# Optimization experiments

Hardware: AMD Instinct MI355X
Metric: run time of the kernel (lower is better)

Reference implementation:

```python
import jax, jax.numpy as jnp
import numpy as np

NUM_CLASSES = 100000
FEAT_DIM = 512
BATCH = 32768
ALPHA1 = 1.0
ALPHA2 = 50.0  # alpha * 50
A_CONST = 0.2
WARMUP = 15
EPS = 1e-12  # torch F.normalize eps


def setup_inputs() -> dict:
    key = jax.random.key(0)
    k1, k2, k3, k4 = jax.random.split(key, 4)
    x = jax.random.normal(k1, (BATCH, FEAT_DIM), dtype=jnp.float32)
    labels = jax.random.randint(k2, (BATCH,), 0, NUM_CLASSES, dtype=jnp.int64)
    ori_labels = jax.random.randint(k3, (BATCH,), 0, NUM_CLASSES, dtype=jnp.int64)
    centers = jax.random.normal(k4, (NUM_CLASSES, FEAT_DIM), dtype=jnp.float32)
    return {"x": x, "labels": labels, "ori_labels": ori_labels, "epoch": 5, "centers": centers}


def _l2norm(v, axis):
    # matches torch F.normalize(p=2): divide by max(||v||, eps)
    n = jnp.sqrt(jnp.sum(v * v, axis=axis, keepdims=True))
    return v / jnp.maximum(n, EPS)


def reference(x, labels, ori_labels, epoch, centers):
    C = centers.shape[0]
    xn = _l2norm(x, axis=1)                      # [B, D]
    cn = _l2norm(centers, axis=1)                # [C, D]

    all_centers_mean = jnp.sum(cn, axis=0) / C   # [D]
    s_all = xn @ all_centers_mean                # [B]  dot(x, mean of all centers)

    # one-hot multiply-and-sum == direct gather of the label's center
    c_lab = cn[labels]                           # [B, D]
    s_lab = jnp.sum(c_lab * xn, axis=1)          # [B]

    e_all = jnp.exp(s_all)
    # first branch scales the gathered center by (C+1)/C before the dot
    loss_1 = jnp.mean((e_all - jnp.exp(s_lab * ((C + 1.0) / C))) / ALPHA1)
    loss_2 = jnp.mean(-jnp.abs((e_all - jnp.exp(s_lab) + A_CONST) / ALPHA2))

    v = min(epoch / (WARMUP - 1), 1)             # epoch is a Python int
    loss = (1.0 - v) * loss_1 + v * loss_2
    return (loss, centers)
```

## Files before the change

### kernel.cpp

```cpp
#include <hip/hip_runtime.h>
#include <math.h>

#define C_CLASSES 100000
#define FEAT      512
#define BATCH_N   32768
#define EPS_N     1e-12f

__global__ void __launch_bounds__(256) centers_pass(
    const float* __restrict__ centers,
    float* __restrict__ out_centers,
    float* __restrict__ cpart,
    float* __restrict__ rnorms)
{
    const int t   = threadIdx.x;
    const int wid = t >> 6;
    const int ln  = t & 63;

    float acc[8] = {0.f,0.f,0.f,0.f,0.f,0.f,0.f,0.f};

    for (int row = blockIdx.x * 4 + wid; row < C_CLASSES; row += gridDim.x * 4) {
        const float* rp = centers + (size_t)row * FEAT;
        float v[8];
        #pragma unroll
        for (int k = 0; k < 8; ++k) v[k] = rp[ln + 64 * k];

        float ss = 0.f;
        #pragma unroll
        for (int k = 0; k < 8; ++k) ss += v[k] * v[k];
        #pragma unroll
        for (int o = 32; o > 0; o >>= 1) ss += __shfl_xor(ss, o, 64);

        const float rn = 1.f / fmaxf(sqrtf(ss), EPS_N);
        if (ln == 0) rnorms[row] = rn;

        #pragma unroll
        for (int k = 0; k < 8; ++k) acc[k] += v[k] * rn;

        float* op = out_centers + (size_t)row * FEAT;
        #pragma unroll
        for (int k = 0; k < 8; ++k) op[ln + 64 * k] = v[k];
    }

    __shared__ float accsh[4][FEAT];
    #pragma unroll
    for (int k = 0; k < 8; ++k) accsh[wid][ln + 64 * k] = acc[k];
    __syncthreads();

    #pragma unroll
    for (int j = t; j < FEAT; j += 256)
        cpart[(size_t)blockIdx.x * FEAT + j] =
            accsh[0][j] + accsh[1][j] + accsh[2][j] + accsh[3][j];
}

__global__ void __launch_bounds__(512) reduce_mean_s1(
    const float* __restrict__ cpart, int nblk,
    float* __restrict__ partial2)
{
    const int j = threadIdx.x;
    float s = 0.f;
    for (int b = blockIdx.x; b < nblk; b += gridDim.x)
        s += cpart[(size_t)b * FEAT + j];
    partial2[(size_t)blockIdx.x * FEAT + j] = s;
}

__global__ void __launch_bounds__(512) reduce_mean_s2(
    const float* __restrict__ partial2, int np,
    float* __restrict__ mean)
{
    const int j = threadIdx.x;
    float s = 0.f;
    for (int p = 0; p < np; ++p)
        s += partial2[(size_t)p * FEAT + j];
    mean[j] = s / (float)C_CLASSES;
}

__global__ void __launch_bounds__(256) row_loss(
    const float* __restrict__ x,
    const int*   __restrict__ labels,
    const float* __restrict__ centers,
    const float* __restrict__ mean,
    const float* __restrict__ rnorms,
    float* __restrict__ lpart)
{
    const int wid = threadIdx.x >> 6;
    const int ln  = threadIdx.x & 63;
    const int row = blockIdx.x * 4 + wid;

    const float4* __restrict__ xr = reinterpret_cast<const float4*>(x + (size_t)row * FEAT);
    const float4* __restrict__ mr = reinterpret_cast<const float4*>(mean);
    const int lab = labels[row];
    const float4* __restrict__ cr = reinterpret_cast<const float4*>(centers + (size_t)lab * FEAT);
    const float rnc = rnorms[lab];

    const float4 xv0 = xr[ln], xv1 = xr[ln + 64];
    const float4 mv0 = mr[ln], mv1 = mr[ln + 64];
    const float4 cv0 = cr[ln], cv1 = cr[ln + 64];

    float ssx = xv0.x*xv0.x + xv0.y*xv0.y + xv0.z*xv0.z + xv0.w*xv0.w
              + xv1.x*xv1.x + xv1.y*xv1.y + xv1.z*xv1.z + xv1.w*xv1.w;
    float dxm = xv0.x*mv0.x + xv0.y*mv0.y + xv0.z*mv0.z + xv0.w*mv0.w
              + xv1.x*mv1.x + xv1.y*mv1.y + xv1.z*mv1.z + xv1.w*mv1.w;
    float dxc = xv0.x*cv0.x + xv0.y*cv0.y + xv0.z*cv0.z + xv0.w*cv0.w
              + xv1.x*cv1.x + xv1.y*cv1.y + xv1.z*cv1.z + xv1.w*cv1.w;

    #pragma unroll
    for (int o = 32; o > 0; o >>= 1) {
        ssx += __shfl_xor(ssx, o, 64);
        dxm += __shfl_xor(dxm, o, 64);
        dxc += __shfl_xor(dxc, o, 64);
    }

    __shared__ float t1s[4], t2s[4];
    if (ln == 0) {
        const float rnx = 1.f / fmaxf(sqrtf(ssx), EPS_N);
        const float s_all = dxm * rnx;
        const float s_lab = dxc * rnx * rnc;
        const float e_all = expf(s_all);
        const float kC    = (float)((double)(C_CLASSES + 1) / (double)C_CLASSES);
        const float t1 = (e_all - expf(s_lab * kC));
        const float t2 = -fabsf((e_all - expf(s_lab) + 0.2f) * (1.f / 50.f));
        t1s[wid] = t1;
        t2s[wid] = t2;
    }
    __syncthreads();
    if (threadIdx.x == 0) {
        lpart[(size_t)blockIdx.x * 2]     = t1s[0] + t1s[1] + t1s[2] + t1s[3];
        lpart[(size_t)blockIdx.x * 2 + 1] = t2s[0] + t2s[1] + t2s[2] + t2s[3];
    }
}

__global__ void final_loss(const float* __restrict__ lpart, int n,
                           const int* __restrict__ epoch,
                           float* __restrict__ out)
{
    __shared__ double sh1[256];
    __shared__ double sh2[256];
    double s1 = 0.0, s2 = 0.0;
    for (int i = threadIdx.x; i < n; i += blockDim.x) {
        s1 += (double)lpart[(size_t)i * 2];
        s2 += (double)lpart[(size_t)i * 2 + 1];
    }
    sh1[threadIdx.x] = s1;
    sh2[threadIdx.x] = s2;
    __syncthreads();
    for (int s = 128; s > 0; s >>= 1) {
        if (threadIdx.x < s) {
            sh1[threadIdx.x] += sh1[threadIdx.x + s];
            sh2[threadIdx.x] += sh2[threadIdx.x + s];
        }
        __syncthreads();
    }
    if (threadIdx.x == 0) {
        const float v  = fminf((float)(*epoch) * (1.f / 14.f), 1.f);
        const float l1 = (float)(sh1[0] / (double)BATCH_N);
        const float l2 = (float)(sh2[0] / (double)BATCH_N);
        out[0] = (1.f - v) * l1 + v * l2;
    }
}

extern "C" void kernel_launch(void* const* d_in, const int* in_sizes, int n_in,
                              void* d_out, int out_size, void* d_ws, size_t ws_size,
                              hipStream_t stream)
{
    const float* x       = (const float*)d_in[0];
    const int*   labels  = (const int*)d_in[1];
    const int*   epoch   = (const int*)d_in[3];
    const float* centers = (const float*)d_in[4];
    float* out = (float*)d_out;

    float* ws       = (float*)d_ws;
    float* mean     = ws;
    float* partial2 = ws + 512;
    float* lpart    = ws + 512 + 16384;
    float* rnorms   = ws + 512 + 16384 + 16384;
    float* cpart    = rnorms + 100352;

    const size_t fixed_bytes = (size_t)(512 + 16384 + 16384 + 100352) * sizeof(float);
    int nblkA = 2048;
    if (ws_size < fixed_bytes + (size_t)nblkA * FEAT * sizeof(float)) {
        size_t avail = (ws_size > fixed_bytes) ? (ws_size - fixed_bytes) : 0;
        nblkA = (int)(avail / (FEAT * sizeof(float)));
        if (nblkA < 1) nblkA = 1;
    }

    centers_pass<<<nblkA, 256, 0, stream>>>(centers, out + 1, cpart, rnorms);
    reduce_mean_s1<<<32, 512, 0, stream>>>(cpart, nblkA, partial2);
    reduce_mean_s2<<<1, 512, 0, stream>>>(partial2, 32, mean);
    row_loss<<<BATCH_N / 4, 256, 0, stream>>>(x, labels, centers, mean, rnorms, lpart);
    final_loss<<<1, 256, 0, stream>>>(lpart, BATCH_N / 4, epoch, out);
}
```

Before: 135.2 us.

## Fuse label-gather dot products into centers pass via block specialization

The centers pass and the x·center(label) work now share one grid: every fifth block handles batch rows, computing the x norm, the label-center norm and their dot product, while the other blocks normalize and copy centers. The later kernel then only reads x and the mean, skipping the random gather of center rows. Center copies use nontemporal stores and the grid size is fixed at 1024 center blocks. Because the x rows are read twice, the data traffic goes up; the intended gain is overlapping the gather with the streaming centers work.

```diff
diff --git a/kernel.cpp b/kernel.cpp
--- a/kernel.cpp
+++ b/kernel.cpp
@@ -6,59 +6,100 @@
 #define BATCH_N   32768
 #define EPS_N     1e-12f
 
-__global__ void __launch_bounds__(256) centers_pass(
+#define NBC   1024
+#define NBX   256
+#define GRID1 1280
+
+__global__ void __launch_bounds__(256) fused_pass(
     const float* __restrict__ centers,
-    float* __restrict__ out_centers,
-    float* __restrict__ cpart,
-    float* __restrict__ rnorms)
+    const float* __restrict__ x,
+    const int*   __restrict__ labels,
+    float*  __restrict__ out_centers,
+    float*  __restrict__ cpart,
+    float2* __restrict__ xscal)
 {
     const int t   = threadIdx.x;
     const int wid = t >> 6;
     const int ln  = t & 63;
-
-    float acc[8] = {0.f,0.f,0.f,0.f,0.f,0.f,0.f,0.f};
-
-    for (int row = blockIdx.x * 4 + wid; row < C_CLASSES; row += gridDim.x * 4) {
-        const float* rp = centers + (size_t)row * FEAT;
-        float v[8];
+    const int bid = blockIdx.x;
+
+    if ((bid % 5) == 4) {
+        const int xb = bid / 5;
+        for (int row = xb * 4 + wid; row < BATCH_N; row += NBX * 4) {
+            const float4* __restrict__ xr =
+                reinterpret_cast<const float4*>(x + (size_t)row * FEAT);
+            const int lab = labels[row];
+            const float4* __restrict__ cr =
+                reinterpret_cast<const float4*>(centers + (size_t)lab * FEAT);
+
+            const float4 xv0 = xr[ln], xv1 = xr[ln + 64];
+            const float4 cv0 = cr[ln], cv1 = cr[ln + 64];
+
+            float ssx = xv0.x*xv0.x + xv0.y*xv0.y + xv0.z*xv0.z + xv0.w*xv0.w
+                      + xv1.x*xv1.x + xv1.y*xv1.y + xv1.z*xv1.z + xv1.w*xv1.w;
+            float dxc = xv0.x*cv0.x + xv0.y*cv0.y + xv0.z*cv0.z + xv0.w*cv0.w
+                      + xv1.x*cv1.x + xv1.y*cv1.y + xv1.z*cv1.z + xv1.w*cv1.w;
+            float ssc = cv0.x*cv0.x + cv0.y*cv0.y + cv0.z*cv0.z + cv0.w*cv0.w
+                      + cv1.x*cv1.x + cv1.y*cv1.y + cv1.z*cv1.z + cv1.w*cv1.w;
+
+            #pragma unroll
+            for (int o = 32; o > 0; o >>= 1) {
+                ssx += __shfl_xor(ssx, o, 64);
+                dxc += __shfl_xor(dxc, o, 64);
+                ssc += __shfl_xor(ssc, o, 64);
+            }
+
+            if (ln == 0) {
+                const float rnx = 1.f / fmaxf(sqrtf(ssx), EPS_N);
+                const float rnc = 1.f / fmaxf(sqrtf(ssc), EPS_N);
+                xscal[row] = make_float2(rnx, dxc * rnx * rnc);
+            }
+        }
+    } else {
+        const int cb = (bid / 5) * 4 + (bid % 5);
+        float acc[8] = {0.f,0.f,0.f,0.f,0.f,0.f,0.f,0.f};
+
+        for (int row = cb * 4 + wid; row < C_CLASSES; row += NBC * 4) {
+            const float* rp = centers + (size_t)row * FEAT;
+            float v[8];
+            #pragma unroll
+            for (int k = 0; k < 8; ++k) v[k] = rp[ln + 64 * k];
+
+            float ss = 0.f;
+            #pragma unroll
+            for (int k = 0; k < 8; ++k) ss += v[k] * v[k];
+            #pragma unroll
+            for (int o = 32; o > 0; o >>= 1) ss += __shfl_xor(ss, o, 64);
+
+            const float rn = 1.f / fmaxf(sqrtf(ss), EPS_N);
+            #pragma unroll
+            for (int k = 0; k < 8; ++k) acc[k] += v[k] * rn;
+
+            float* op = out_centers + (size_t)row * FEAT;
+            #pragma unroll
+            for (int k = 0; k < 8; ++k)
+                __builtin_nontemporal_store(v[k], &op[ln + 64 * k]);
+        }
+
+        __shared__ float accsh[4][FEAT];
         #pragma unroll
-        for (int k = 0; k < 8; ++k) v[k] = rp[ln + 64 * k];
-
-        float ss = 0.f;
+        for (int k = 0; k < 8; ++k) accsh[wid][ln + 64 * k] = acc[k];
+        __syncthreads();
+
         #pragma unroll
-        for (int k = 0; k < 8; ++k) ss += v[k] * v[k];
-        #pragma unroll
-        for (int o = 32; o > 0; o >>= 1) ss += __shfl_xor(ss, o, 64);
-
-        const float rn = 1.f / fmaxf(sqrtf(ss), EPS_N);
-        if (ln == 0) rnorms[row] = rn;
-
-        #pragma unroll
-        for (int k = 0; k < 8; ++k) acc[k] += v[k] * rn;
-
-        float* op = out_centers + (size_t)row * FEAT;
-        #pragma unroll
-        for (int k = 0; k < 8; ++k) op[ln + 64 * k] = v[k];
-    }
-
-    __shared__ float accsh[4][FEAT];
-    #pragma unroll
-    for (int k = 0; k < 8; ++k) accsh[wid][ln + 64 * k] = acc[k];
-    __syncthreads();
-
-    #pragma unroll
-    for (int j = t; j < FEAT; j += 256)
-        cpart[(size_t)blockIdx.x * FEAT + j] =
-            accsh[0][j] + accsh[1][j] + accsh[2][j] + accsh[3][j];
+        for (int j = t; j < FEAT; j += 256)
+            cpart[(size_t)cb * FEAT + j] =
+                accsh[0][j] + accsh[1][j] + accsh[2][j] + accsh[3][j];
+    }
 }
 
 __global__ void __launch_bounds__(512) reduce_mean_s1(
-    const float* __restrict__ cpart, int nblk,
+    const float* __restrict__ cpart,
     float* __restrict__ partial2)
 {
     const int j = threadIdx.x;
     float s = 0.f;
-    for (int b = blockIdx.x; b < nblk; b += gridDim.x)
+    for (int b = blockIdx.x; b < NBC; b += gridDim.x)
         s += cpart[(size_t)b * FEAT + j];
     partial2[(size_t)blockIdx.x * FEAT + j] = s;
 }
@@ -74,12 +115,10 @@
     mean[j] = s / (float)C_CLASSES;
 }
 
-__global__ void __launch_bounds__(256) row_loss(
-    const float* __restrict__ x,
-    const int*   __restrict__ labels,
-    const float* __restrict__ centers,
-    const float* __restrict__ mean,
-    const float* __restrict__ rnorms,
+__global__ void __launch_bounds__(256) xmean_finish(
+    const float*  __restrict__ x,
+    const float*  __restrict__ mean,
+    const float2* __restrict__ xscal,
     float* __restrict__ lpart)
 {
     const int wid = threadIdx.x >> 6;
@@ -88,33 +127,22 @@
 
     const float4* __restrict__ xr = reinterpret_cast<const float4*>(x + (size_t)row * FEAT);
     const float4* __restrict__ mr = reinterpret_cast<const float4*>(mean);
-    const int lab = labels[row];
-    const float4* __restrict__ cr = reinterpret_cast<const float4*>(centers + (size_t)lab * FEAT);
-    const float rnc = rnorms[lab];
 
     const float4 xv0 = xr[ln], xv1 = xr[ln + 64];
     const float4 mv0 = mr[ln], mv1 = mr[ln + 64];
-    const float4 cv0 = cr[ln], cv1 = cr[ln + 64];
-
-    float ssx = xv0.x*xv0.x + xv0.y*xv0.y + xv0.z*xv0.z + xv0.w*xv0.w
-              + xv1.x*xv1.x + xv1.y*xv1.y + xv1.z*xv1.z + xv1.w*xv1.w;
+
     float dxm = xv0.x*mv0.x + xv0.y*mv0.y + xv0.z*mv0.z + xv0.w*mv0.w
               + xv1.x*mv1.x + xv1.y*mv1.y + xv1.z*mv1.z + xv1.w*mv1.w;
-    float dxc = xv0.x*cv0.x + xv0.y*cv0.y + xv0.z*cv0.z + xv0.w*cv0.w
-              + xv1.x*cv1.x + xv1.y*cv1.y + xv1.z*cv1.z + xv1.w*cv1.w;
 
     #pragma unroll
-    for (int o = 32; o > 0; o >>= 1) {
-        ssx += __shfl_xor(ssx, o, 64);
-        dxm += __shfl_xor(dxm, o, 64);
-        dxc += __shfl_xor(dxc, o, 64);
-    }
+    for (int o = 32; o > 0; o >>= 1) dxm += __shfl_xor(dxm, o, 64);
 
     __shared__ float t1s[4], t2s[4];
     if (ln == 0) {
-        const float rnx = 1.f / fmaxf(sqrtf(ssx), EPS_N);
+        const float2 sc   = xscal[row];
+        const float rnx   = sc.x;
+        const float s_lab = sc.y;
         const float s_all = dxm * rnx;
-        const float s_lab = dxc * rnx * rnc;
         const float e_all = expf(s_all);
         const float kC    = (float)((double)(C_CLASSES + 1) / (double)C_CLASSES);
         const float t1 = (e_all - expf(s_lab * kC));
@@ -168,24 +196,16 @@
     const float* centers = (const float*)d_in[4];
     float* out = (float*)d_out;
 
-    float* ws       = (float*)d_ws;
-    float* mean     = ws;
-    float* partial2 = ws + 512;
-    float* lpart    = ws + 512 + 16384;
-    float* rnorms   = ws + 512 + 16384 + 16384;
-    float* cpart    = rnorms + 100352;
-
-    const size_t fixed_bytes = (size_t)(512 + 16384 + 16384 + 100352) * sizeof(float);
-    int nblkA = 2048;
-    if (ws_size < fixed_bytes + (size_t)nblkA * FEAT * sizeof(float)) {
-        size_t avail = (ws_size > fixed_bytes) ? (ws_size - fixed_bytes) : 0;
-        nblkA = (int)(avail / (FEAT * sizeof(float)));
-        if (nblkA < 1) nblkA = 1;
-    }
-
-    centers_pass<<<nblkA, 256, 0, stream>>>(centers, out + 1, cpart, rnorms);
-    reduce_mean_s1<<<32, 512, 0, stream>>>(cpart, nblkA, partial2);
+    float*  ws       = (float*)d_ws;
+    float*  mean     = ws;
+    float*  partial2 = ws + 512;
+    float*  lpart    = ws + 512 + 16384;
+    float2* xscal    = (float2*)(ws + 512 + 16384 + 16384);
+    float*  cpart    = ws + 512 + 16384 + 16384 + 65536;
+
+    fused_pass<<<GRID1, 256, 0, stream>>>(centers, x, labels, out + 1, cpart, xscal);
+    reduce_mean_s1<<<32, 512, 0, stream>>>(cpart, partial2);
     reduce_mean_s2<<<1, 512, 0, stream>>>(partial2, 32, mean);
-    row_loss<<<BATCH_N / 4, 256, 0, stream>>>(x, labels, centers, mean, rnorms, lpart);
+    xmean_finish<<<BATCH_N / 4, 256, 0, stream>>>(x, mean, xscal, lpart);
     final_loss<<<1, 256, 0, stream>>>(lpart, BATCH_N / 4, epoch, out);
 }
```

Measured after the change: 135.8 us. No clear change (+0.4%).

## Fuse all stages into one cooperative kernel with grid-wide syncs

Applied to the files above, without the earlier changes.

Replaces the five separate kernel launches with a single cooperative kernel whose phases are separated by grid.sync(), with a multi-launch fallback when cooperative launch fails. It also drops the per-class rnorms buffer and recomputes the gathered center's norm inside the row-loss phase. The row phase becomes grid-strided over persistent blocks. The aim is to remove launch gaps and tail effects. In exchange it adds grid-barrier cost, and the recomputed norm is an extra reduction per row.

```diff
diff --git a/kernel.cpp b/kernel.cpp
--- a/kernel.cpp
+++ b/kernel.cpp
@@ -1,160 +1,172 @@
 #include <hip/hip_runtime.h>
+#include <hip/hip_cooperative_groups.h>
 #include <math.h>
+
+namespace cg = cooperative_groups;
 
 #define C_CLASSES 100000
 #define FEAT      512
 #define BATCH_N   32768
 #define EPS_N     1e-12f
 
-__global__ void __launch_bounds__(256) centers_pass(
+__global__ void __launch_bounds__(256) rdc_coop(
+    const float* __restrict__ x,
+    const int*   __restrict__ labels,
+    const int*   __restrict__ epoch,
     const float* __restrict__ centers,
-    float* __restrict__ out_centers,
-    float* __restrict__ cpart,
-    float* __restrict__ rnorms)
+    float*       __restrict__ out,
+    float*       __restrict__ cpart,
+    float*       __restrict__ partial2,
+    float*       __restrict__ lpart,
+    int phase_lo, int phase_hi, int coop)
 {
     const int t   = threadIdx.x;
     const int wid = t >> 6;
     const int ln  = t & 63;
-
-    float acc[8] = {0.f,0.f,0.f,0.f,0.f,0.f,0.f,0.f};
-
-    for (int row = blockIdx.x * 4 + wid; row < C_CLASSES; row += gridDim.x * 4) {
-        const float* rp = centers + (size_t)row * FEAT;
-        float v[8];
+    const int bid = blockIdx.x;
+    const int nb  = gridDim.x;
+
+    __shared__ float accsh[4][FEAT];
+    __shared__ float mean_sh[FEAT];
+    __shared__ float redsh[2][4];
+    __shared__ double dsh1[256];
+    __shared__ double dsh2[256];
+
+    if (phase_lo <= 0 && 0 < phase_hi) {
+        float4 a0 = make_float4(0.f,0.f,0.f,0.f);
+        float4 a1 = make_float4(0.f,0.f,0.f,0.f);
+        float* outc = out + 1;
+
+        for (int row = bid * 4 + wid; row < C_CLASSES; row += nb * 4) {
+            const float4* rp = reinterpret_cast<const float4*>(centers + (size_t)row * FEAT);
+            const float4 v0 = rp[ln];
+            const float4 v1 = rp[ln + 64];
+
+            float ss = v0.x*v0.x + v0.y*v0.y + v0.z*v0.z + v0.w*v0.w
+                     + v1.x*v1.x + v1.y*v1.y + v1.z*v1.z + v1.w*v1.w;
+            #pragma unroll
+            for (int o = 32; o > 0; o >>= 1) ss += __shfl_xor(ss, o, 64);
+
+            const float rn = 1.f / fmaxf(sqrtf(ss), EPS_N);
+            a0.x += v0.x * rn; a0.y += v0.y * rn; a0.z += v0.z * rn; a0.w += v0.w * rn;
+            a1.x += v1.x * rn; a1.y += v1.y * rn; a1.z += v1.z * rn; a1.w += v1.w * rn;
+
+            float* op = outc + (size_t)row * FEAT;
+            op[4*ln + 0] = v0.x; op[4*ln + 1] = v0.y;
+            op[4*ln + 2] = v0.z; op[4*ln + 3] = v0.w;
+            op[256 + 4*ln + 0] = v1.x; op[256 + 4*ln + 1] = v1.y;
+            op[256 + 4*ln + 2] = v1.z; op[256 + 4*ln + 3] = v1.w;
+        }
+
+        accsh[wid][4*ln + 0] = a0.x; accsh[wid][4*ln + 1] = a0.y;
+        accsh[wid][4*ln + 2] = a0.z; accsh[wid][4*ln + 3] = a0.w;
+        accsh[wid][256 + 4*ln + 0] = a1.x; accsh[wid][256 + 4*ln + 1] = a1.y;
+        accsh[wid][256 + 4*ln + 2] = a1.z; accsh[wid][256 + 4*ln + 3] = a1.w;
+        __syncthreads();
+
         #pragma unroll
-        for (int k = 0; k < 8; ++k) v[k] = rp[ln + 64 * k];
-
-        float ss = 0.f;
-        #pragma unroll
-        for (int k = 0; k < 8; ++k) ss += v[k] * v[k];
-        #pragma unroll
-        for (int o = 32; o > 0; o >>= 1) ss += __shfl_xor(ss, o, 64);
-
-        const float rn = 1.f / fmaxf(sqrtf(ss), EPS_N);
-        if (ln == 0) rnorms[row] = rn;
-
-        #pragma unroll
-        for (int k = 0; k < 8; ++k) acc[k] += v[k] * rn;
-
-        float* op = out_centers + (size_t)row * FEAT;
-        #pragma unroll
-        for (int k = 0; k < 8; ++k) op[ln + 64 * k] = v[k];
-    }
-
-    __shared__ float accsh[4][FEAT];
-    #pragma unroll
-    for (int k = 0; k < 8; ++k) accsh[wid][ln + 64 * k] = acc[k];
-    __syncthreads();
-
-    #pragma unroll
-    for (int j = t; j < FEAT; j += 256)
-        cpart[(size_t)blockIdx.x * FEAT + j] =
-            accsh[0][j] + accsh[1][j] + accsh[2][j] + accsh[3][j];
-}
-
-__global__ void __launch_bounds__(512) reduce_mean_s1(
-    const float* __restrict__ cpart, int nblk,
-    float* __restrict__ partial2)
-{
-    const int j = threadIdx.x;
-    float s = 0.f;
-    for (int b = blockIdx.x; b < nblk; b += gridDim.x)
-        s += cpart[(size_t)b * FEAT + j];
-    partial2[(size_t)blockIdx.x * FEAT + j] = s;
-}
-
-__global__ void __launch_bounds__(512) reduce_mean_s2(
-    const float* __restrict__ partial2, int np,
-    float* __restrict__ mean)
-{
-    const int j = threadIdx.x;
-    float s = 0.f;
-    for (int p = 0; p < np; ++p)
-        s += partial2[(size_t)p * FEAT + j];
-    mean[j] = s / (float)C_CLASSES;
-}
-
-__global__ void __launch_bounds__(256) row_loss(
-    const float* __restrict__ x,
-    const int*   __restrict__ labels,
-    const float* __restrict__ centers,
-    const float* __restrict__ mean,
-    const float* __restrict__ rnorms,
-    float* __restrict__ lpart)
-{
-    const int wid = threadIdx.x >> 6;
-    const int ln  = threadIdx.x & 63;
-    const int row = blockIdx.x * 4 + wid;
-
-    const float4* __restrict__ xr = reinterpret_cast<const float4*>(x + (size_t)row * FEAT);
-    const float4* __restrict__ mr = reinterpret_cast<const float4*>(mean);
-    const int lab = labels[row];
-    const float4* __restrict__ cr = reinterpret_cast<const float4*>(centers + (size_t)lab * FEAT);
-    const float rnc = rnorms[lab];
-
-    const float4 xv0 = xr[ln], xv1 = xr[ln + 64];
-    const float4 mv0 = mr[ln], mv1 = mr[ln + 64];
-    const float4 cv0 = cr[ln], cv1 = cr[ln + 64];
-
-    float ssx = xv0.x*xv0.x + xv0.y*xv0.y + xv0.z*xv0.z + xv0.w*xv0.w
-              + xv1.x*xv1.x + xv1.y*xv1.y + xv1.z*xv1.z + xv1.w*xv1.w;
-    float dxm = xv0.x*mv0.x + xv0.y*mv0.y + xv0.z*mv0.z + xv0.w*mv0.w
-              + xv1.x*mv1.x + xv1.y*mv1.y + xv1.z*mv1.z + xv1.w*mv1.w;
-    float dxc = xv0.x*cv0.x + xv0.y*cv0.y + xv0.z*cv0.z + xv0.w*cv0.w
-              + xv1.x*cv1.x + xv1.y*cv1.y + xv1.z*cv1.z + xv1.w*cv1.w;
-
-    #pragma unroll
-    for (int o = 32; o > 0; o >>= 1) {
-        ssx += __shfl_xor(ssx, o, 64);
-        dxm += __shfl_xor(dxm, o, 64);
-        dxc += __shfl_xor(dxc, o, 64);
-    }
-
-    __shared__ float t1s[4], t2s[4];
-    if (ln == 0) {
-        const float rnx = 1.f / fmaxf(sqrtf(ssx), EPS_N);
-        const float s_all = dxm * rnx;
-        const float s_lab = dxc * rnx * rnc;
-        const float e_all = expf(s_all);
-        const float kC    = (float)((double)(C_CLASSES + 1) / (double)C_CLASSES);
-        const float t1 = (e_all - expf(s_lab * kC));
-        const float t2 = -fabsf((e_all - expf(s_lab) + 0.2f) * (1.f / 50.f));
-        t1s[wid] = t1;
-        t2s[wid] = t2;
-    }
-    __syncthreads();
-    if (threadIdx.x == 0) {
-        lpart[(size_t)blockIdx.x * 2]     = t1s[0] + t1s[1] + t1s[2] + t1s[3];
-        lpart[(size_t)blockIdx.x * 2 + 1] = t2s[0] + t2s[1] + t2s[2] + t2s[3];
-    }
-}
-
-__global__ void final_loss(const float* __restrict__ lpart, int n,
-                           const int* __restrict__ epoch,
-                           float* __restrict__ out)
-{
-    __shared__ double sh1[256];
-    __shared__ double sh2[256];
-    double s1 = 0.0, s2 = 0.0;
-    for (int i = threadIdx.x; i < n; i += blockDim.x) {
-        s1 += (double)lpart[(size_t)i * 2];
-        s2 += (double)lpart[(size_t)i * 2 + 1];
-    }
-    sh1[threadIdx.x] = s1;
-    sh2[threadIdx.x] = s2;
-    __syncthreads();
-    for (int s = 128; s > 0; s >>= 1) {
-        if (threadIdx.x < s) {
-            sh1[threadIdx.x] += sh1[threadIdx.x + s];
-            sh2[threadIdx.x] += sh2[threadIdx.x + s];
+        for (int j = t; j < FEAT; j += 256)
+            cpart[(size_t)bid * FEAT + j] =
+                accsh[0][j] + accsh[1][j] + accsh[2][j] + accsh[3][j];
+    }
+
+    if (coop && phase_lo <= 0 && 1 < phase_hi) cg::this_grid().sync();
+
+    if (phase_lo <= 1 && 1 < phase_hi) {
+        if (bid < 32) {
+            for (int j = t; j < FEAT; j += 256) {
+                float s = 0.f;
+                for (int b = bid; b < nb; b += 32)
+                    s += cpart[(size_t)b * FEAT + j];
+                partial2[(size_t)bid * FEAT + j] = s;
+            }
+        }
+    }
+
+    if (coop && phase_lo <= 1 && 2 < phase_hi) cg::this_grid().sync();
+
+    if (phase_lo <= 2 && 2 < phase_hi) {
+        for (int j = t; j < FEAT; j += 256) {
+            float s = 0.f;
+            #pragma unroll
+            for (int p = 0; p < 32; ++p) s += partial2[(size_t)p * FEAT + j];
+            mean_sh[j] = s * (1.f / (float)C_CLASSES);
         }
         __syncthreads();
-    }
-    if (threadIdx.x == 0) {
-        const float v  = fminf((float)(*epoch) * (1.f / 14.f), 1.f);
-        const float l1 = (float)(sh1[0] / (double)BATCH_N);
-        const float l2 = (float)(sh2[0] / (double)BATCH_N);
-        out[0] = (1.f - v) * l1 + v * l2;
+
+        const float4 mv0 = *reinterpret_cast<const float4*>(&mean_sh[4*ln]);
+        const float4 mv1 = *reinterpret_cast<const float4*>(&mean_sh[256 + 4*ln]);
+
+        float t1acc = 0.f, t2acc = 0.f;
+        const float kC = (float)((double)(C_CLASSES + 1) / (double)C_CLASSES);
+
+        for (int row = bid * 4 + wid; row < BATCH_N; row += nb * 4) {
+            const float4* xr = reinterpret_cast<const float4*>(x + (size_t)row * FEAT);
+            const int lab = labels[row];
+            const float4* cr = reinterpret_cast<const float4*>(centers + (size_t)lab * FEAT);
+
+            const float4 xv0 = xr[ln], xv1 = xr[ln + 64];
+            const float4 cv0 = cr[ln], cv1 = cr[ln + 64];
+
+            float ssx = xv0.x*xv0.x + xv0.y*xv0.y + xv0.z*xv0.z + xv0.w*xv0.w
+                      + xv1.x*xv1.x + xv1.y*xv1.y + xv1.z*xv1.z + xv1.w*xv1.w;
+            float dxm = xv0.x*mv0.x + xv0.y*mv0.y + xv0.z*mv0.z + xv0.w*mv0.w
+                      + xv1.x*mv1.x + xv1.y*mv1.y + xv1.z*mv1.z + xv1.w*mv1.w;
+            float dxc = xv0.x*cv0.x + xv0.y*cv0.y + xv0.z*cv0.z + xv0.w*cv0.w
+                      + xv1.x*cv1.x + xv1.y*cv1.y + xv1.z*cv1.z + xv1.w*cv1.w;
+            float ssc = cv0.x*cv0.x + cv0.y*cv0.y + cv0.z*cv0.z + cv0.w*cv0.w
+                      + cv1.x*cv1.x + cv1.y*cv1.y + cv1.z*cv1.z + cv1.w*cv1.w;
+
+            #pragma unroll
+            for (int o = 32; o > 0; o >>= 1) {
+                ssx += __shfl_xor(ssx, o, 64);
+                dxm += __shfl_xor(dxm, o, 64);
+                dxc += __shfl_xor(dxc, o, 64);
+                ssc += __shfl_xor(ssc, o, 64);
+            }
+
+            if (ln == 0) {
+                const float rnx = 1.f / fmaxf(sqrtf(ssx), EPS_N);
+                const float rnc = 1.f / fmaxf(sqrtf(ssc), EPS_N);
+                const float s_all = dxm * rnx;
+                const float s_lab = dxc * rnx * rnc;
+                const float e_all = expf(s_all);
+                t1acc += (e_all - expf(s_lab * kC));
+                t2acc += -fabsf((e_all - expf(s_lab) + 0.2f) * (1.f / 50.f));
+            }
+        }
+
+        if (ln == 0) { redsh[0][wid] = t1acc; redsh[1][wid] = t2acc; }
+        __syncthreads();
+        if (t == 0) {
+            lpart[(size_t)bid * 2]     = redsh[0][0] + redsh[0][1] + redsh[0][2] + redsh[0][3];
+            lpart[(size_t)bid * 2 + 1] = redsh[1][0] + redsh[1][1] + redsh[1][2] + redsh[1][3];
+        }
+    }
+
+    if (coop && phase_lo <= 2 && 3 < phase_hi) cg::this_grid().sync();
+
+    if (phase_lo <= 3 && 3 < phase_hi) {
+        if (bid == 0) {
+            double s1 = 0.0, s2 = 0.0;
+            for (int i = t; i < nb; i += 256) {
+                s1 += (double)lpart[(size_t)i * 2];
+                s2 += (double)lpart[(size_t)i * 2 + 1];
+            }
+            dsh1[t] = s1;
+            dsh2[t] = s2;
+            __syncthreads();
+            for (int s = 128; s > 0; s >>= 1) {
+                if (t < s) { dsh1[t] += dsh1[t + s]; dsh2[t] += dsh2[t + s]; }
+                __syncthreads();
+            }
+            if (t == 0) {
+                const float v  = fminf((float)(*epoch) * (1.f / 14.f), 1.f);
+                const float l1 = (float)(dsh1[0] / (double)BATCH_N);
+                const float l2 = (float)(dsh2[0] / (double)BATCH_N);
+                out[0] = (1.f - v) * l1 + v * l2;
+            }
+        }
     }
 }
 
@@ -169,23 +181,33 @@
     float* out = (float*)d_out;
 
     float* ws       = (float*)d_ws;
-    float* mean     = ws;
-    float* partial2 = ws + 512;
-    float* lpart    = ws + 512 + 16384;
-    float* rnorms   = ws + 512 + 16384 + 16384;
-    float* cpart    = rnorms + 100352;
-
-    const size_t fixed_bytes = (size_t)(512 + 16384 + 16384 + 100352) * sizeof(float);
-    int nblkA = 2048;
-    if (ws_size < fixed_bytes + (size_t)nblkA * FEAT * sizeof(float)) {
-        size_t avail = (ws_size > fixed_bytes) ? (ws_size - fixed_bytes) : 0;
-        nblkA = (int)(avail / (FEAT * sizeof(float)));
-        if (nblkA < 1) nblkA = 1;
-    }
-
-    centers_pass<<<nblkA, 256, 0, stream>>>(centers, out + 1, cpart, rnorms);
-    reduce_mean_s1<<<32, 512, 0, stream>>>(cpart, nblkA, partial2);
-    reduce_mean_s2<<<1, 512, 0, stream>>>(partial2, 32, mean);
-    row_loss<<<BATCH_N / 4, 256, 0, stream>>>(x, labels, centers, mean, rnorms, lpart);
-    final_loss<<<1, 256, 0, stream>>>(lpart, BATCH_N / 4, epoch, out);
+    float* partial2 = ws;
+    float* lpart    = ws + 16384;
+    float* cpart    = ws + 16384 + 8192;
+
+    int maxb = 0;
+    hipError_t oe = hipOccupancyMaxActiveBlocksPerMultiprocessor(&maxb, rdc_coop, 256, 0);
+    if (oe != hipSuccess || maxb < 1) maxb = 4;
+    int grid = maxb * 256;
+    if (grid > 2048) grid = 2048;
+    if (grid < 64)   grid = 64;
+
+    int pl0 = 0, ph4 = 4, coop1 = 1;
+    void* args[] = {
+        (void*)&x, (void*)&labels, (void*)&epoch, (void*)&centers,
+        (void*)&out, (void*)&cpart, (void*)&partial2, (void*)&lpart,
+        (void*)&pl0, (void*)&ph4, (void*)&coop1
+    };
+    hipError_t le = hipLaunchCooperativeKernel((const void*)rdc_coop,
+                                               dim3(grid), dim3(256), args, 0, stream);
+    if (le != hipSuccess) {
+        rdc_coop<<<grid, 256, 0, stream>>>(x, labels, epoch, centers, out,
+                                           cpart, partial2, lpart, 0, 1, 0);
+        rdc_coop<<<grid, 256, 0, stream>>>(x, labels, epoch, centers, out,
+                                           cpart, partial2, lpart, 1, 2, 0);
+        rdc_coop<<<grid, 256, 0, stream>>>(x, labels, epoch, centers, out,
+                                           cpart, partial2, lpart, 2, 3, 0);
+        rdc_coop<<<grid, 256, 0, stream>>>(x, labels, epoch, centers, out,
+                                           cpart, partial2, lpart, 3, 4, 0);
+    }
 }
```

Result: slower. 476.0 us (+252.0%).
